# Performance work log

Measured on AMD Instinct MI355X. Metric: run time of the kernel, lower is better.

The kernel has to match this reference:

```python
import jax, jax.numpy as jnp
import numpy as np

N_NODES = 100000
N_EDGES = 3200000
IN_DIM = 256
OUT_DIM = 128


def setup_inputs() -> dict:
    key = jax.random.key(0)
    k1, k2, k3, k4, k5 = jax.random.split(key, 5)
    # node features
    x = jax.random.normal(k1, (N_NODES, IN_DIM), dtype=jnp.float32)
    # glorot-uniform weight as in glorot_init
    init_range = np.sqrt(6.0 / (IN_DIM + OUT_DIM)).astype(np.float32)
    weight = jax.random.uniform(k2, (IN_DIM, OUT_DIM), dtype=jnp.float32,
                                minval=-init_range, maxval=init_range)
    # sparse adjacency in COO form: adj[dst, src] = edge_weight
    edge_src = jax.random.randint(k3, (N_EDGES,), 0, N_NODES, dtype=jnp.int64)
    edge_dst = jax.random.randint(k4, (N_EDGES,), 0, N_NODES, dtype=jnp.int64)
    edge_weight = jax.random.uniform(k5, (N_EDGES,), dtype=jnp.float32)
    return {"x": x, "weight": weight, "edge_weight": edge_weight,
            "edge_src": edge_src, "edge_dst": edge_dst}


def reference(x, weight, edge_weight, edge_src, edge_dst):
    # dense feature transform: [N, in] @ [in, out] -> [N, out]
    xw = x @ weight
    # sparse adjacency matmul (adj @ xw) as gather + weighted scatter-add
    msgs = xw[edge_src] * edge_weight[:, None]           # [E, out]
    agg = jax.ops.segment_sum(msgs, edge_dst, num_segments=N_NODES)
    # fused activation
    return jax.nn.relu(agg)
```

## Files before the change

### kernel.cpp

```cpp
#include <hip/hip_runtime.h>

#define IN_DIM 256
#define OUT_DIM 128
#define BMG 128
#define BKG 64

#define BSHIFT 7
#define BNODES 128
#define MAXB2 832
#define EPT1 10
#define CHUNK1 2560
#define CAPB 4736
#define HCAP 2560
#define RPT 19

typedef __attribute__((ext_vector_type(4))) float floatx4;
typedef __attribute__((ext_vector_type(8))) short shortx8;

static __device__ __forceinline__ unsigned short f2bf(float f) {
  unsigned u = __float_as_uint(f);
  u += 0x7FFFu + ((u >> 16) & 1u);
  return (unsigned short)(u >> 16);
}

__global__ __launch_bounds__(256) void prep_kernel(
    const float* __restrict__ w, unsigned short* __restrict__ wt,
    int* __restrict__ btail, int nb2) {
  const int idx = blockIdx.x * 256 + threadIdx.x;
  const int k = idx >> 7;
  const int n = idx & 127;
  wt[n * IN_DIM + k] = f2bf(w[idx]);
  if (blockIdx.x == 0)
    for (int b = threadIdx.x; b < nb2; b += 256) btail[b] = 0;
}

__global__ __launch_bounds__(256) void fused_pg_kernel(
    const float* __restrict__ x, const unsigned short* __restrict__ wt,
    unsigned short* __restrict__ xw, int n_nodes,
    const int* __restrict__ esrc, const int* __restrict__ edst,
    const float* __restrict__ ew, int* __restrict__ btail,
    uint2* __restrict__ csr2, int n_edges, int nb2, int pblocks) {
  __shared__ __align__(16) union {
    struct {
      unsigned short As[BMG][BKG + 8];
      unsigned short Bs[OUT_DIM][BKG + 8];
    } g;
    struct {
      uint2 srec[CHUNK1];
      int hcnt[MAXB2];
      int aux[MAXB2];
      int sh[256];
    } p;
  } sm;

  const int bid = blockIdx.x;
  const int P = pblocks;
  const int G = (int)gridDim.x - pblocks;
  bool is_part;
  int vb;
  if (P <= G) {
    if (bid < 2 * P) { is_part = !(bid & 1); vb = bid >> 1; }
    else             { is_part = false;      vb = bid - P; }
  } else {
    if (bid < 2 * G) { is_part = (bid & 1);  vb = bid >> 1; }
    else             { is_part = true;       vb = bid - G; }
  }

  const int t = threadIdx.x;

  if (is_part) {
    const int base = vb * CHUNK1;
    const int cn = min(CHUNK1, n_edges - base);

    for (int b = t; b < MAXB2; b += 256) sm.p.hcnt[b] = 0;
    __syncthreads();

    int dst[EPT1];
    unsigned xpk[EPT1];
#pragma unroll
    for (int i = 0; i < EPT1; ++i) {
      const int idx = t + i * 256;
      if (idx < cn) {
        const int e = base + idx;
        dst[i] = edst[e];
        unsigned wb = __float_as_uint(ew[e]);
        wb += 0x7FFFu + ((wb >> 16) & 1u);
        xpk[i] = ((wb >> 16) << 17) | (unsigned)esrc[e];
        atomicAdd(&sm.p.hcnt[((unsigned)dst[i]) >> BSHIFT], 1);
      } else {
        dst[i] = -1;
      }
    }
    __syncthreads();
    {
      const int b4 = 4 * t;
      int a0 = 0, a1 = 0, a2 = 0, a3 = 0;
      if (b4 < MAXB2) {
        a0 = sm.p.hcnt[b4];     a1 = sm.p.hcnt[b4 + 1];
        a2 = sm.p.hcnt[b4 + 2]; a3 = sm.p.hcnt[b4 + 3];
      }
      const int s = a0 + a1 + a2 + a3;
      sm.p.sh[t] = s;
      __syncthreads();
      for (int off = 1; off < 256; off <<= 1) {
        const int add = (t >= off) ? sm.p.sh[t - off] : 0;
        __syncthreads();
        sm.p.sh[t] += add;
        __syncthreads();
      }
      if (b4 < MAXB2) {
        int run = sm.p.sh[t] - s;
        sm.p.aux[b4] = run; run += a0;
        sm.p.aux[b4 + 1] = run; run += a1;
        sm.p.aux[b4 + 2] = run; run += a2;
        sm.p.aux[b4 + 3] = run;
      }
    }
    __syncthreads();
    for (int b = t; b < nb2; b += 256) {
      const int c = sm.p.hcnt[b];
      const int lo = sm.p.aux[b];
      int g = 0;
      if (c) g = b * CAPB + atomicAdd(&btail[b], c);
      sm.p.hcnt[b] = lo;
      sm.p.aux[b] = g - lo;
    }
    __syncthreads();
#pragma unroll
    for (int i = 0; i < EPT1; ++i)
      if (dst[i] >= 0) {
        const int bk = ((unsigned)dst[i]) >> BSHIFT;
        const int p = atomicAdd(&sm.p.hcnt[bk], 1);
        sm.p.srec[p] = make_uint2(xpk[i], (unsigned)dst[i]);
      }
    __syncthreads();
    for (int i = t; i < cn; i += 256) {
      const uint2 r = sm.p.srec[i];
      const int bk = r.y >> BSHIFT;
      const size_t pos = (size_t)(sm.p.aux[bk] + i);
      if (pos < (size_t)(bk + 1) * CAPB) csr2[pos] = r;
    }
  } else {
    const int wv = t >> 6;
    const int wr = wv >> 1;
    const int wc = wv & 1;
    const int lane = t & 63;
    const int quad = lane >> 4;
    const int l16 = lane & 15;
    const int row0 = vb * BMG;
    if (row0 >= n_nodes) return;

    floatx4 acc[4][4];
#pragma unroll
    for (int a = 0; a < 4; ++a)
#pragma unroll
      for (int b = 0; b < 4; ++b) acc[a][b] = (floatx4){0.f, 0.f, 0.f, 0.f};

    for (int k0 = 0; k0 < IN_DIM; k0 += BKG) {
      __syncthreads();
#pragma unroll
      for (int i = 0; i < 8; ++i) {
        const int idx = i * 256 + t;
        const int r = idx >> 4;
        const int kq = (idx & 15) * 4;
        int row = row0 + r;
        if (row >= n_nodes) row = n_nodes - 1;
        const float4 v = *(const float4*)(x + (size_t)row * IN_DIM + k0 + kq);
        ushort4 sv;
        sv.x = f2bf(v.x); sv.y = f2bf(v.y); sv.z = f2bf(v.z); sv.w = f2bf(v.w);
        *(ushort4*)&sm.g.As[r][kq] = sv;
      }
#pragma unroll
      for (int i = 0; i < 4; ++i) {
        const int idx16 = i * 256 + t;
        const int n = idx16 >> 3;
        const int off = (idx16 & 7) * 8;
        *(int4*)&sm.g.Bs[n][off] =
            *(const int4*)(wt + (size_t)n * IN_DIM + k0 + off);
      }
      __syncthreads();

#pragma unroll
      for (int kk = 0; kk < BKG; kk += 32) {
        shortx8 af[4];
#pragma unroll
        for (int tm = 0; tm < 4; ++tm)
          af[tm] =
              *(const shortx8*)&sm.g.As[wr * 64 + tm * 16 + l16][kk + quad * 8];
        shortx8 bfr[4];
#pragma unroll
        for (int tn = 0; tn < 4; ++tn)
          bfr[tn] =
              *(const shortx8*)&sm.g.Bs[wc * 64 + tn * 16 + l16][kk + quad * 8];
#pragma unroll
        for (int tm = 0; tm < 4; ++tm)
#pragma unroll
          for (int tn = 0; tn < 4; ++tn)
            acc[tm][tn] = __builtin_amdgcn_mfma_f32_16x16x32_bf16(
                af[tm], bfr[tn], acc[tm][tn], 0, 0, 0);
      }
    }

#pragma unroll
    for (int tm = 0; tm < 4; ++tm)
#pragma unroll
      for (int tn = 0; tn < 4; ++tn)
#pragma unroll
        for (int r = 0; r < 4; ++r) {
          const int grow = row0 + wr * 64 + tm * 16 + quad * 4 + r;
          const int gcol = wc * 64 + tn * 16 + l16;
          if (grow < n_nodes)
            xw[(size_t)grow * OUT_DIM + gcol] = f2bf(acc[tm][tn][r]);
        }
  }
}

struct AggSmem {
  unsigned xs[HCAP];
  int cnt[64];
  int cur[64];
  int sst[64];
  int sen[64];
  int sh[64];
};

__global__ __launch_bounds__(256, 4) void sort_agg_kernel(
    const uint2* __restrict__ csr2, const int* __restrict__ btail,
    const unsigned short* __restrict__ xw, float* __restrict__ out,
    int n_nodes) {
  __shared__ __align__(16) AggSmem sm;
  const int t = threadIdx.x;

  const int nwg = (int)gridDim.x;
  const int q = nwg >> 3, r = nwg & 7;
  const int xcd = blockIdx.x & 7, bix = blockIdx.x >> 3;
  const int lb = (xcd < r ? xcd * (q + 1) : r * (q + 1) + (xcd - r) * q) + bix;

  const int bucket = lb >> 1;
  const int half = lb & 1;
  const int node0 = (bucket << BSHIFT) + half * 64;
  const size_t S = (size_t)bucket * CAPB;
  const int cnt = min(btail[bucket], CAPB);

  uint2 rec[RPT];
#pragma unroll
  for (int k = 0; k < RPT; ++k) {
    const int i = t + k * 256;
    rec[k] = (i < cnt) ? csr2[S + i] : make_uint2(0u, 0xFFFFFFFFu);
  }

  if (t < 64) sm.cnt[t] = 0;
  __syncthreads();
#pragma unroll
  for (int k = 0; k < RPT; ++k) {
    const unsigned y = rec[k].y;
    if (y != 0xFFFFFFFFu) {
      const unsigned yl = y & (BNODES - 1);
      if ((int)(yl >> 6) == half) atomicAdd(&sm.cnt[yl & 63], 1);
    }
  }
  __syncthreads();
  {
    const int s = (t < 64) ? sm.cnt[t] : 0;
    if (t < 64) sm.sh[t] = s;
    __syncthreads();
    for (int off = 1; off < 64; off <<= 1) {
      const int add = (t >= off && t < 64) ? sm.sh[t - off] : 0;
      __syncthreads();
      if (t < 64) sm.sh[t] += add;
      __syncthreads();
    }
    if (t < 64) {
      const int run = sm.sh[t] - s;
      sm.cur[t] = run;
      sm.sst[t] = run;
      sm.sen[t] = run + s;
    }
  }
  __syncthreads();
#pragma unroll
  for (int k = 0; k < RPT; ++k) {
    const uint2 rr = rec[k];
    if (rr.y != 0xFFFFFFFFu) {
      const unsigned yl = rr.y & (BNODES - 1);
      if ((int)(yl >> 6) == half) {
        const int p = atomicAdd(&sm.cur[yl & 63], 1);
        if (p < HCAP) sm.xs[p] = rr.x;
      }
    }
  }
  if (t < 64) sm.sh[t] = ((sm.sen[t] - sm.sst[t]) << 6) | t;
  __syncthreads();
  for (int kk = 2; kk <= 64; kk <<= 1) {
    for (int jj = kk >> 1; jj > 0; jj >>= 1) {
      if (t < 64) {
        const int ixj = t ^ jj;
        if (ixj > t) {
          const int a = sm.sh[t], b = sm.sh[ixj];
          const bool up = ((t & kk) == 0);
          if ((a > b) == up) { sm.sh[t] = b; sm.sh[ixj] = a; }
        }
      }
      __syncthreads();
    }
  }

  const int g = t >> 4;
  const int lane = t & 15;
  const int d8 = lane * 8;
  const unsigned short* __restrict__ xwd = xw + d8;

#pragma unroll
  for (int ii = 0; ii < 4; ++ii) {
    const int nl = sm.sh[g + (ii << 4)] & 63;
    const int node = node0 + nl;
    if (node >= n_nodes) continue;
    const int j0 = sm.sst[nl];
    const int j1 = min(sm.sen[nl], HCAP);

    float a0 = 0.f, a1 = 0.f, a2 = 0.f, a3 = 0.f;
    float a4 = 0.f, a5 = 0.f, a6 = 0.f, a7 = 0.f;

    int j = j0;
    const int n8 = (j1 - j0) & ~7;
    if (n8 > 0) {
      uint4 v[8];
      float wq[8];
#pragma unroll
      for (int u = 0; u < 8; ++u) {
        const unsigned p = sm.xs[j0 + u];
        v[u] = *(const uint4*)(xwd + (size_t)(p & 0x1FFFFu) * OUT_DIM);
        wq[u] = __uint_as_float((p >> 17) << 16);
      }
      for (j = j0 + 8; j < j0 + n8; j += 8) {
        uint4 nv[8];
        float nw[8];
#pragma unroll
        for (int u = 0; u < 8; ++u) {
          const unsigned p = sm.xs[j + u];
          nv[u] = *(const uint4*)(xwd + (size_t)(p & 0x1FFFFu) * OUT_DIM);
          nw[u] = __uint_as_float((p >> 17) << 16);
        }
#pragma unroll
        for (int u = 0; u < 8; ++u) {
          a0 = fmaf(__uint_as_float(v[u].x << 16), wq[u], a0);
          a1 = fmaf(__uint_as_float(v[u].x & 0xFFFF0000u), wq[u], a1);
          a2 = fmaf(__uint_as_float(v[u].y << 16), wq[u], a2);
          a3 = fmaf(__uint_as_float(v[u].y & 0xFFFF0000u), wq[u], a3);
          a4 = fmaf(__uint_as_float(v[u].z << 16), wq[u], a4);
          a5 = fmaf(__uint_as_float(v[u].z & 0xFFFF0000u), wq[u], a5);
          a6 = fmaf(__uint_as_float(v[u].w << 16), wq[u], a6);
          a7 = fmaf(__uint_as_float(v[u].w & 0xFFFF0000u), wq[u], a7);
        }
#pragma unroll
        for (int u = 0; u < 8; ++u) {
          v[u] = nv[u];
          wq[u] = nw[u];
        }
      }
#pragma unroll
      for (int u = 0; u < 8; ++u) {
        a0 = fmaf(__uint_as_float(v[u].x << 16), wq[u], a0);
        a1 = fmaf(__uint_as_float(v[u].x & 0xFFFF0000u), wq[u], a1);
        a2 = fmaf(__uint_as_float(v[u].y << 16), wq[u], a2);
        a3 = fmaf(__uint_as_float(v[u].y & 0xFFFF0000u), wq[u], a3);
        a4 = fmaf(__uint_as_float(v[u].z << 16), wq[u], a4);
        a5 = fmaf(__uint_as_float(v[u].z & 0xFFFF0000u), wq[u], a5);
        a6 = fmaf(__uint_as_float(v[u].w << 16), wq[u], a6);
        a7 = fmaf(__uint_as_float(v[u].w & 0xFFFF0000u), wq[u], a7);
      }
      j = j0 + n8;
    }
    for (; j < j1; ++j) {
      const unsigned p0 = sm.xs[j];
      const float w0 = __uint_as_float((p0 >> 17) << 16);
      const uint4 v0 = *(const uint4*)(xwd + (size_t)(p0 & 0x1FFFFu) * OUT_DIM);
      a0 = fmaf(__uint_as_float(v0.x << 16), w0, a0);
      a1 = fmaf(__uint_as_float(v0.x & 0xFFFF0000u), w0, a1);
      a2 = fmaf(__uint_as_float(v0.y << 16), w0, a2);
      a3 = fmaf(__uint_as_float(v0.y & 0xFFFF0000u), w0, a3);
      a4 = fmaf(__uint_as_float(v0.z << 16), w0, a4);
      a5 = fmaf(__uint_as_float(v0.z & 0xFFFF0000u), w0, a5);
      a6 = fmaf(__uint_as_float(v0.w << 16), w0, a6);
      a7 = fmaf(__uint_as_float(v0.w & 0xFFFF0000u), w0, a7);
    }

    float4 o0, o1;
    o0.x = fmaxf(a0, 0.f); o0.y = fmaxf(a1, 0.f);
    o0.z = fmaxf(a2, 0.f); o0.w = fmaxf(a3, 0.f);
    o1.x = fmaxf(a4, 0.f); o1.y = fmaxf(a5, 0.f);
    o1.z = fmaxf(a6, 0.f); o1.w = fmaxf(a7, 0.f);
    float* orow = out + (size_t)node * OUT_DIM + d8;
    *(float4*)orow = o0;
    *(float4*)(orow + 4) = o1;
  }
}

extern "C" void kernel_launch(void* const* d_in, const int* in_sizes, int n_in,
                              void* d_out, int out_size, void* d_ws,
                              size_t ws_size, hipStream_t stream) {
  const float* x    = (const float*)d_in[0];
  const float* w    = (const float*)d_in[1];
  const float* ew   = (const float*)d_in[2];
  const int*   esrc = (const int*)d_in[3];
  const int*   edst = (const int*)d_in[4];
  float* out = (float*)d_out;

  const int n_edges = in_sizes[2];
  const int n_nodes = out_size / OUT_DIM;
  const int nb2 = (n_nodes + BNODES - 1) >> BSHIFT;

  char* p = (char*)d_ws;
  unsigned short* xw = (unsigned short*)p;
  p += (size_t)n_nodes * OUT_DIM * sizeof(unsigned short);
  p = (char*)(((uintptr_t)p + 15) & ~(uintptr_t)15);
  unsigned short* wt = (unsigned short*)p;
  p += (size_t)OUT_DIM * IN_DIM * sizeof(unsigned short);
  p = (char*)(((uintptr_t)p + 15) & ~(uintptr_t)15);
  uint2* csr2 = (uint2*)p;  p += (size_t)nb2 * CAPB * sizeof(uint2);
  int* btail = (int*)p;     p += (size_t)nb2 * sizeof(int);

  prep_kernel<<<(IN_DIM * OUT_DIM) / 256, 256, 0, stream>>>(w, wt, btail, nb2);

  const int pblocks = (n_edges + CHUNK1 - 1) / CHUNK1;
  const int gblocks = (n_nodes + BMG - 1) / BMG;
  fused_pg_kernel<<<pblocks + gblocks, 256, 0, stream>>>(
      x, wt, xw, n_nodes, esrc, edst, ew, btail, csr2, n_edges, nb2, pblocks);

  sort_agg_kernel<<<2 * nb2, 256, 0, stream>>>(csr2, btail, xw, out, n_nodes);
}
```

Baseline: 336.4 us.

## Process whole 128-node bucket per 512-thread block instead of two halves

New measurement: 343.8 us. 1.02x slower.

```diff
diff --git a/kernel.cpp b/kernel.cpp
--- a/kernel.cpp
+++ b/kernel.cpp
@@ -11,8 +11,7 @@
 #define EPT1 10
 #define CHUNK1 2560
 #define CAPB 4736
-#define HCAP 2560
-#define RPT 19
+#define RPT 10
 
 typedef __attribute__((ext_vector_type(4))) float floatx4;
 typedef __attribute__((ext_vector_type(8))) short shortx8;
@@ -216,15 +215,15 @@
 }
 
 struct AggSmem {
-  unsigned xs[HCAP];
-  int cnt[64];
-  int cur[64];
-  int sst[64];
-  int sen[64];
-  int sh[64];
+  unsigned xs[CAPB];
+  int cnt[BNODES];
+  int cur[BNODES];
+  int sst[BNODES];
+  int sen[BNODES];
+  int sh[BNODES];
 };
 
-__global__ __launch_bounds__(256, 4) void sort_agg_kernel(
+__global__ __launch_bounds__(512) void sort_agg_kernel(
     const uint2* __restrict__ csr2, const int* __restrict__ btail,
     const unsigned short* __restrict__ xw, float* __restrict__ out,
     int n_nodes) {
@@ -234,43 +233,39 @@
   const int nwg = (int)gridDim.x;
   const int q = nwg >> 3, r = nwg & 7;
   const int xcd = blockIdx.x & 7, bix = blockIdx.x >> 3;
-  const int lb = (xcd < r ? xcd * (q + 1) : r * (q + 1) + (xcd - r) * q) + bix;
-
-  const int bucket = lb >> 1;
-  const int half = lb & 1;
-  const int node0 = (bucket << BSHIFT) + half * 64;
+  const int bucket =
+      (xcd < r ? xcd * (q + 1) : r * (q + 1) + (xcd - r) * q) + bix;
+
+  const int node0 = bucket << BSHIFT;
   const size_t S = (size_t)bucket * CAPB;
   const int cnt = min(btail[bucket], CAPB);
 
   uint2 rec[RPT];
 #pragma unroll
   for (int k = 0; k < RPT; ++k) {
-    const int i = t + k * 256;
+    const int i = t + k * 512;
     rec[k] = (i < cnt) ? csr2[S + i] : make_uint2(0u, 0xFFFFFFFFu);
   }
 
-  if (t < 64) sm.cnt[t] = 0;
+  if (t < BNODES) sm.cnt[t] = 0;
   __syncthreads();
 #pragma unroll
   for (int k = 0; k < RPT; ++k) {
     const unsigned y = rec[k].y;
-    if (y != 0xFFFFFFFFu) {
-      const unsigned yl = y & (BNODES - 1);
-      if ((int)(yl >> 6) == half) atomicAdd(&sm.cnt[yl & 63], 1);
-    }
+    if (y != 0xFFFFFFFFu) atomicAdd(&sm.cnt[y & (BNODES - 1)], 1);
   }
   __syncthreads();
   {
-    const int s = (t < 64) ? sm.cnt[t] : 0;
-    if (t < 64) sm.sh[t] = s;
-    __syncthreads();
-    for (int off = 1; off < 64; off <<= 1) {
-      const int add = (t >= off && t < 64) ? sm.sh[t - off] : 0;
-      __syncthreads();
-      if (t < 64) sm.sh[t] += add;
-      __syncthreads();
-    }
-    if (t < 64) {
+    const int s = (t < BNODES) ? sm.cnt[t] : 0;
+    if (t < BNODES) sm.sh[t] = s;
+    __syncthreads();
+    for (int off = 1; off < BNODES; off <<= 1) {
+      const int add = (t >= off && t < BNODES) ? sm.sh[t - off] : 0;
+      __syncthreads();
+      if (t < BNODES) sm.sh[t] += add;
+      __syncthreads();
+    }
+    if (t < BNODES) {
       const int run = sm.sh[t] - s;
       sm.cur[t] = run;
       sm.sst[t] = run;
@@ -282,18 +277,15 @@
   for (int k = 0; k < RPT; ++k) {
     const uint2 rr = rec[k];
     if (rr.y != 0xFFFFFFFFu) {
-      const unsigned yl = rr.y & (BNODES - 1);
-      if ((int)(yl >> 6) == half) {
-        const int p = atomicAdd(&sm.cur[yl & 63], 1);
-        if (p < HCAP) sm.xs[p] = rr.x;
-      }
-    }
-  }
-  if (t < 64) sm.sh[t] = ((sm.sen[t] - sm.sst[t]) << 6) | t;
+      const int p = atomicAdd(&sm.cur[rr.y & (BNODES - 1)], 1);
+      if (p < CAPB) sm.xs[p] = rr.x;
+    }
+  }
+  if (t < BNODES) sm.sh[t] = ((sm.sen[t] - sm.sst[t]) << BSHIFT) | t;
   __syncthreads();
-  for (int kk = 2; kk <= 64; kk <<= 1) {
+  for (int kk = 2; kk <= BNODES; kk <<= 1) {
     for (int jj = kk >> 1; jj > 0; jj >>= 1) {
-      if (t < 64) {
+      if (t < BNODES) {
         const int ixj = t ^ jj;
         if (ixj > t) {
           const int a = sm.sh[t], b = sm.sh[ixj];
@@ -312,11 +304,11 @@
 
 #pragma unroll
   for (int ii = 0; ii < 4; ++ii) {
-    const int nl = sm.sh[g + (ii << 4)] & 63;
+    const int nl = sm.sh[g + (ii << 5)] & (BNODES - 1);
     const int node = node0 + nl;
     if (node >= n_nodes) continue;
     const int j0 = sm.sst[nl];
-    const int j1 = min(sm.sen[nl], HCAP);
+    const int j1 = min(sm.sen[nl], CAPB);
 
     float a0 = 0.f, a1 = 0.f, a2 = 0.f, a3 = 0.f;
     float a4 = 0.f, a5 = 0.f, a6 = 0.f, a7 = 0.f;
@@ -427,5 +419,5 @@
   fused_pg_kernel<<<pblocks + gblocks, 256, 0, stream>>>(
       x, wt, xw, n_nodes, esrc, edst, ew, btail, csr2, n_edges, nb2, pblocks);
 
-  sort_agg_kernel<<<2 * nb2, 256, 0, stream>>>(csr2, btail, xw, out, n_nodes);
+  sort_agg_kernel<<<nb2, 512, 0, stream>>>(csr2, btail, xw, out, n_nodes);
 }
```
